# Kernel optimization log

Hardware: AMD Instinct MI355X
Metric: run time of the kernel (lower is better)

The kernel has to match this reference:

```python
import jax, jax.numpy as jnp
import numpy as np

NT, NM, E, EL = 400000, 40000, 400000, 1000000
C, H = 64, 64  # node_embedding_channels, hidden_channels
F_T = 384      # thesis feature dim


def setup_inputs() -> dict:
    key = jax.random.key(0)
    ks = jax.random.split(key, 24)
    s = 1.0 / np.sqrt(C)
    inp = {
        "x_thesis": jax.random.normal(ks[0], (NT, F_T), jnp.float32),
        "thesis_node_id": jnp.arange(NT, dtype=jnp.int32),
        "mentor_node_id": jnp.arange(NM, dtype=jnp.int32),
        "edge_src": jax.random.randint(ks[1], (E,), 0, NT, jnp.int32),
        "edge_dst": jax.random.randint(ks[2], (E,), 0, NM, jnp.int32),
        "el_src": jax.random.randint(ks[3], (EL,), 0, NT, jnp.int32),
        "el_dst": jax.random.randint(ks[4], (EL,), 0, NM, jnp.int32),
        "lin_W": jax.random.normal(ks[5], (C, F_T), jnp.float32) / np.sqrt(F_T),
        "lin_b": jnp.zeros((C,), jnp.float32),
        "emb_t": jax.random.normal(ks[6], (NT, C), jnp.float32),
        "emb_m": jax.random.normal(ks[7], (NM, C), jnp.float32),
        # SAGEConv params per layer per edge type (tm: thesis->mentor, mt: mentor->thesis)
        "Wl_tm0": jax.random.normal(ks[8], (H, C), jnp.float32) * s,
        "Wr_tm0": jax.random.normal(ks[9], (H, C), jnp.float32) * s,
        "b_tm0": jnp.zeros((H,), jnp.float32),
        "Wl_mt0": jax.random.normal(ks[10], (H, C), jnp.float32) * s,
        "Wr_mt0": jax.random.normal(ks[11], (H, C), jnp.float32) * s,
        "b_mt0": jnp.zeros((H,), jnp.float32),
        "Wl_tm1": jax.random.normal(ks[12], (H, H), jnp.float32) * s,
        "Wr_tm1": jax.random.normal(ks[13], (H, H), jnp.float32) * s,
        "b_tm1": jnp.zeros((H,), jnp.float32),
        "Wl_mt1": jax.random.normal(ks[14], (H, H), jnp.float32) * s,
        "Wr_mt1": jax.random.normal(ks[15], (H, H), jnp.float32) * s,
        "b_mt1": jnp.zeros((H,), jnp.float32),
    }
    return inp


def _segment_mean(msgs, seg_ids, num_segments):
    summed = jax.ops.segment_sum(msgs, seg_ids, num_segments=num_segments)
    cnt = jax.ops.segment_sum(jnp.ones((msgs.shape[0],), msgs.dtype), seg_ids,
                              num_segments=num_segments)
    return summed / jnp.maximum(cnt, 1.0)[:, None]


def _sage_layer(x_t, x_m, edge_src, edge_dst,
                Wl_tm, Wr_tm, b_tm, Wl_mt, Wr_mt, b_mt):
    # thesis -> mentor: mean-aggregate thesis neighbors at each mentor
    agg_m = _segment_mean(x_t[edge_src], edge_dst, x_m.shape[0])
    out_m = agg_m @ Wl_tm.T + x_m @ Wr_tm.T + b_tm
    # mentor -> thesis (reverse edges): mean-aggregate mentor neighbors at each thesis
    agg_t = _segment_mean(x_m[edge_dst], edge_src, x_t.shape[0])
    out_t = agg_t @ Wl_mt.T + x_t @ Wr_mt.T + b_mt
    return out_t, out_m


def reference(x_thesis, thesis_node_id, mentor_node_id, edge_src, edge_dst,
              el_src, el_dst, lin_W, lin_b, emb_t, emb_m,
              Wl_tm0, Wr_tm0, b_tm0, Wl_mt0, Wr_mt0, b_mt0,
              Wl_tm1, Wr_tm1, b_tm1, Wl_mt1, Wr_mt1, b_mt1):
    # node encoders
    x_t = x_thesis @ lin_W.T + lin_b + emb_t[thesis_node_id]
    x_m = emb_m[mentor_node_id]
    # 2-layer hetero GraphSAGE (ReLU between layers, none after last)
    x_t, x_m = _sage_layer(x_t, x_m, edge_src, edge_dst,
                           Wl_tm0, Wr_tm0, b_tm0, Wl_mt0, Wr_mt0, b_mt0)
    x_t, x_m = jax.nn.relu(x_t), jax.nn.relu(x_m)
    x_t, x_m = _sage_layer(x_t, x_m, edge_src, edge_dst,
                           Wl_tm1, Wr_tm1, b_tm1, Wl_mt1, Wr_mt1, b_mt1)
    # edge dot-product classifier over label edges
    return jnp.sum(x_t[el_src] * x_m[el_dst], axis=-1)
```

## Files before the change

kernel.cpp:

```cpp
#include <hip/hip_runtime.h>
#include <hip/hip_bf16.h>
#include <cstdint>
#include <cstddef>

#define TILE_BM 64
#define TILE_BN 64
#define TILE_BK 32

__global__ __launch_bounds__(256)
void encoder_kernel(const float* __restrict__ X, int K,
                    const float* __restrict__ W,
                    const float* __restrict__ bias,
                    const int* __restrict__ ids,
                    const float* __restrict__ emb,
                    float* __restrict__ out, int M)
{
    __shared__ float As[TILE_BK][TILE_BM + 4];
    __shared__ float Bs[TILE_BK][TILE_BN + 4];
    const int tid  = threadIdx.x;
    const int row0 = blockIdx.x * TILE_BM;
    const int tr   = tid >> 4;
    const int tc   = tid & 15;

    float acc[4][4];
#pragma unroll
    for (int i = 0; i < 4; i++)
#pragma unroll
        for (int j = 0; j < 4; j++) acc[i][j] = 0.f;

    for (int k0 = 0; k0 < K; k0 += TILE_BK) {
#pragma unroll
        for (int i = 0; i < 2; i++) {
            int idx = tid + i * 256;
            int r = idx >> 3;
            int j = idx & 7;
            int gr = row0 + r;
            float4 v = make_float4(0.f, 0.f, 0.f, 0.f);
            if (gr < M) v = *(const float4*)&X[(size_t)gr * K + k0 + j * 4];
            As[j * 4 + 0][r] = v.x; As[j * 4 + 1][r] = v.y;
            As[j * 4 + 2][r] = v.z; As[j * 4 + 3][r] = v.w;
        }
#pragma unroll
        for (int i = 0; i < 2; i++) {
            int idx = tid + i * 256;
            int c = idx >> 3;
            int j = idx & 7;
            float4 v = *(const float4*)&W[(size_t)c * K + k0 + j * 4];
            Bs[j * 4 + 0][c] = v.x; Bs[j * 4 + 1][c] = v.y;
            Bs[j * 4 + 2][c] = v.z; Bs[j * 4 + 3][c] = v.w;
        }
        __syncthreads();
#pragma unroll
        for (int kk = 0; kk < TILE_BK; kk++) {
            float4 av = *(const float4*)&As[kk][tr * 4];
            float4 bv = *(const float4*)&Bs[kk][tc * 4];
            float a_[4] = {av.x, av.y, av.z, av.w};
            float b_[4] = {bv.x, bv.y, bv.z, bv.w};
#pragma unroll
            for (int i = 0; i < 4; i++)
#pragma unroll
                for (int j = 0; j < 4; j++) acc[i][j] += a_[i] * b_[j];
        }
        __syncthreads();
    }

    float4 bv = *(const float4*)&bias[tc * 4];
#pragma unroll
    for (int i = 0; i < 4; i++) {
        int r = row0 + tr * 4 + i;
        if (r >= M) continue;
        int id = ids[r];
        float4 ev = *(const float4*)&emb[(size_t)id * 64 + tc * 4];
        float4 o;
        o.x = acc[i][0] + bv.x + ev.x;
        o.y = acc[i][1] + bv.y + ev.y;
        o.z = acc[i][2] + bv.z + ev.z;
        o.w = acc[i][3] + bv.w + ev.w;
        *(float4*)&out[(size_t)r * 64 + tc * 4] = o;
    }
}

__global__ __launch_bounds__(256)
void sage_linear_kernel(const float* __restrict__ A0, const float* __restrict__ W0,
                        const float* __restrict__ A1, const float* __restrict__ W1,
                        const float* __restrict__ bias, float* __restrict__ out,
                        int M, int relu)
{
    __shared__ float As[TILE_BK][TILE_BM + 4];
    __shared__ float Bs[TILE_BK][TILE_BN + 4];
    const int tid  = threadIdx.x;
    const int row0 = blockIdx.x * TILE_BM;
    const int tr   = tid >> 4;
    const int tc   = tid & 15;

    float acc[4][4];
#pragma unroll
    for (int i = 0; i < 4; i++)
#pragma unroll
        for (int j = 0; j < 4; j++) acc[i][j] = 0.f;

    for (int phase = 0; phase < 2; phase++) {
        const float* A = phase ? A1 : A0;
        const float* W = phase ? W1 : W0;
        for (int k0 = 0; k0 < 64; k0 += TILE_BK) {
#pragma unroll
            for (int i = 0; i < 2; i++) {
                int idx = tid + i * 256;
                int r = idx >> 3;
                int j = idx & 7;
                int gr = row0 + r;
                float4 v = make_float4(0.f, 0.f, 0.f, 0.f);
                if (gr < M) v = *(const float4*)&A[(size_t)gr * 64 + k0 + j * 4];
                As[j * 4 + 0][r] = v.x; As[j * 4 + 1][r] = v.y;
                As[j * 4 + 2][r] = v.z; As[j * 4 + 3][r] = v.w;
            }
#pragma unroll
            for (int i = 0; i < 2; i++) {
                int idx = tid + i * 256;
                int c = idx >> 3;
                int j = idx & 7;
                float4 v = *(const float4*)&W[(size_t)c * 64 + k0 + j * 4];
                Bs[j * 4 + 0][c] = v.x; Bs[j * 4 + 1][c] = v.y;
                Bs[j * 4 + 2][c] = v.z; Bs[j * 4 + 3][c] = v.w;
            }
            __syncthreads();
#pragma unroll
            for (int kk = 0; kk < TILE_BK; kk++) {
                float4 av = *(const float4*)&As[kk][tr * 4];
                float4 bv = *(const float4*)&Bs[kk][tc * 4];
                float a_[4] = {av.x, av.y, av.z, av.w};
                float b_[4] = {bv.x, bv.y, bv.z, bv.w};
#pragma unroll
                for (int i = 0; i < 4; i++)
#pragma unroll
                    for (int j = 0; j < 4; j++) acc[i][j] += a_[i] * b_[j];
            }
            __syncthreads();
        }
    }

    float4 bv = *(const float4*)&bias[tc * 4];
#pragma unroll
    for (int i = 0; i < 4; i++) {
        int r = row0 + tr * 4 + i;
        if (r >= M) continue;
        float4 o;
        o.x = acc[i][0] + bv.x;
        o.y = acc[i][1] + bv.y;
        o.z = acc[i][2] + bv.z;
        o.w = acc[i][3] + bv.w;
        if (relu) {
            o.x = fmaxf(o.x, 0.f); o.y = fmaxf(o.y, 0.f);
            o.z = fmaxf(o.z, 0.f); o.w = fmaxf(o.w, 0.f);
        }
        *(float4*)&out[(size_t)r * 64 + tc * 4] = o;
    }
}

__global__ void deg_kernel(const int* __restrict__ src, const int* __restrict__ dst,
                           float* __restrict__ deg_t, float* __restrict__ deg_m, int E)
{
    int e = blockIdx.x * 256 + threadIdx.x;
    if (e < E) {
        atomicAdd(&deg_t[src[e]], 1.f);
        atomicAdd(&deg_m[dst[e]], 1.f);
    }
}

__global__ void inv_kernel(float* __restrict__ d, int n)
{
    int i = blockIdx.x * 256 + threadIdx.x;
    if (i < n) d[i] = 1.f / fmaxf(d[i], 1.f);
}

__global__ void gather_rows_kernel(const float* __restrict__ src, const int* __restrict__ ids,
                                   float* __restrict__ out, int M)
{
    int gid = blockIdx.x * 256 + threadIdx.x;
    int r = gid >> 4;
    int j = gid & 15;
    if (r < M) {
        *(float4*)&out[(size_t)r * 64 + j * 4] =
            *(const float4*)&src[(size_t)ids[r] * 64 + j * 4];
    }
}

__global__ __launch_bounds__(256)
void scatter_kernel(const float* __restrict__ feat, const int* __restrict__ idx_from,
                    const int* __restrict__ idx_to, const float* __restrict__ inv_deg,
                    float* __restrict__ agg, int E)
{
    int gid = blockIdx.x * 256 + threadIdx.x;
    int e = gid >> 6;
    int c = gid & 63;
    if (e < E) {
        int f = idx_from[e];
        int t = idx_to[e];
        float v = feat[(size_t)f * 64 + c] * inv_deg[t];
        atomicAdd(&agg[(size_t)t * 64 + c], v);
    }
}

__global__ __launch_bounds__(256)
void classify_kernel(const float* __restrict__ xt, const float* __restrict__ xm,
                     const int* __restrict__ es, const int* __restrict__ ed,
                     float* __restrict__ out, int EL)
{
    int gid = blockIdx.x * 256 + threadIdx.x;
    int g = gid >> 4;
    int j = gid & 15;
    if (g < EL) {
        int s = es[g];
        int d = ed[g];
        float4 a = *(const float4*)&xt[(size_t)s * 64 + j * 4];
        float4 b = *(const float4*)&xm[(size_t)d * 64 + j * 4];
        float v = a.x * b.x + a.y * b.y + a.z * b.z + a.w * b.w;
        v += __shfl_down(v, 8, 16);
        v += __shfl_down(v, 4, 16);
        v += __shfl_down(v, 2, 16);
        v += __shfl_down(v, 1, 16);
        if (j == 0) out[g] = v;
    }
}

extern "C" void kernel_launch(void* const* d_in, const int* in_sizes, int n_in,
                              void* d_out, int out_size, void* d_ws, size_t ws_size,
                              hipStream_t stream)
{
    const float* x_thesis  = (const float*)d_in[0];
    const int*   thesis_id = (const int*)d_in[1];
    const int*   mentor_id = (const int*)d_in[2];
    const int*   edge_src  = (const int*)d_in[3];
    const int*   edge_dst  = (const int*)d_in[4];
    const int*   el_src    = (const int*)d_in[5];
    const int*   el_dst    = (const int*)d_in[6];
    const float* lin_W     = (const float*)d_in[7];
    const float* lin_b     = (const float*)d_in[8];
    const float* emb_t     = (const float*)d_in[9];
    const float* emb_m     = (const float*)d_in[10];
    const float* Wl_tm0    = (const float*)d_in[11];
    const float* Wr_tm0    = (const float*)d_in[12];
    const float* b_tm0     = (const float*)d_in[13];
    const float* Wl_mt0    = (const float*)d_in[14];
    const float* Wr_mt0    = (const float*)d_in[15];
    const float* b_mt0     = (const float*)d_in[16];
    const float* Wl_tm1    = (const float*)d_in[17];
    const float* Wr_tm1    = (const float*)d_in[18];
    const float* b_tm1     = (const float*)d_in[19];
    const float* Wl_mt1    = (const float*)d_in[20];
    const float* Wr_mt1    = (const float*)d_in[21];
    const float* b_mt1     = (const float*)d_in[22];

    const int NT = in_sizes[1];
    const int NM = in_sizes[2];
    const int E  = in_sizes[3];
    const int EL = in_sizes[5];
    const int FT = in_sizes[0] / NT;

    char* ws = (char*)d_ws;
    size_t off = 0;
    auto alloc = [&](size_t bytes) -> void* {
        void* p = ws + off;
        off += (bytes + 255) & ~(size_t)255;
        return p;
    };
    float* xt_a  = (float*)alloc((size_t)NT * 64 * 4);
    float* xt_b  = (float*)alloc((size_t)NT * 64 * 4);
    float* agg_t = (float*)alloc((size_t)NT * 64 * 4);
    float* xm_a  = (float*)alloc((size_t)NM * 64 * 4);
    float* xm_b  = (float*)alloc((size_t)NM * 64 * 4);
    float* agg_m = (float*)alloc((size_t)NM * 64 * 4);
    float* deg_t = (float*)alloc((size_t)NT * 4);
    float* deg_m = (float*)alloc((size_t)NM * 4);
    (void)ws_size; (void)n_in; (void)out_size;

    hipMemsetAsync(deg_t, 0, (size_t)NT * 4, stream);
    hipMemsetAsync(deg_m, 0, (size_t)NM * 4, stream);
    deg_kernel<<<(E + 255) / 256, 256, 0, stream>>>(edge_src, edge_dst, deg_t, deg_m, E);
    inv_kernel<<<(NT + 255) / 256, 256, 0, stream>>>(deg_t, NT);
    inv_kernel<<<(NM + 255) / 256, 256, 0, stream>>>(deg_m, NM);

    encoder_kernel<<<(NT + 63) / 64, 256, 0, stream>>>(x_thesis, FT, lin_W, lin_b,
                                                       thesis_id, emb_t, xt_a, NT);
    gather_rows_kernel<<<(NM * 16 + 255) / 256, 256, 0, stream>>>(emb_m, mentor_id, xm_a, NM);

    const int scatter_grid = (int)(((size_t)E * 64 + 255) / 256);

    hipMemsetAsync(agg_m, 0, (size_t)NM * 64 * 4, stream);
    hipMemsetAsync(agg_t, 0, (size_t)NT * 64 * 4, stream);
    scatter_kernel<<<scatter_grid, 256, 0, stream>>>(xt_a, edge_src, edge_dst, deg_m, agg_m, E);
    scatter_kernel<<<scatter_grid, 256, 0, stream>>>(xm_a, edge_dst, edge_src, deg_t, agg_t, E);
    sage_linear_kernel<<<(NM + 63) / 64, 256, 0, stream>>>(agg_m, Wl_tm0, xm_a, Wr_tm0,
                                                           b_tm0, xm_b, NM, 1);
    sage_linear_kernel<<<(NT + 63) / 64, 256, 0, stream>>>(agg_t, Wl_mt0, xt_a, Wr_mt0,
                                                           b_mt0, xt_b, NT, 1);

    hipMemsetAsync(agg_m, 0, (size_t)NM * 64 * 4, stream);
    hipMemsetAsync(agg_t, 0, (size_t)NT * 64 * 4, stream);
    scatter_kernel<<<scatter_grid, 256, 0, stream>>>(xt_b, edge_src, edge_dst, deg_m, agg_m, E);
    scatter_kernel<<<scatter_grid, 256, 0, stream>>>(xm_b, edge_dst, edge_src, deg_t, agg_t, E);
    sage_linear_kernel<<<(NM + 63) / 64, 256, 0, stream>>>(agg_m, Wl_tm1, xm_b, Wr_tm1,
                                                           b_tm1, xm_a, NM, 0);
    sage_linear_kernel<<<(NT + 63) / 64, 256, 0, stream>>>(agg_t, Wl_mt1, xt_b, Wr_mt1,
                                                           b_mt1, xt_a, NT, 0);

    classify_kernel<<<(int)(((size_t)EL * 16 + 255) / 256), 256, 0, stream>>>(
        xt_a, xm_a, el_src, el_dst, (float*)d_out, EL);
}
```

Baseline: 1.713 ms.

## Replace atomic scatter aggregation with CSR build and pull-based gather

Builds CSR adjacency for both directions (integer degree count, three-pass prefix scan, atomic-cursor fill), then computes each segment mean by having each destination row gather and sum its neighbours' features. This removes the per-element float atomics of the scatter kernels and the memsets of the aggregation buffers, and it folds the mean division into the gather. The cost is several extra small kernels and extra workspace for the CSR. Neighbour order inside a segment is nondeterministic, so the float summation order can vary between runs.

```diff
diff --git a/kernel.cpp b/kernel.cpp
--- a/kernel.cpp
+++ b/kernel.cpp
@@ -6,6 +6,7 @@
 #define TILE_BM 64
 #define TILE_BN 64
 #define TILE_BK 32
+#define SCAN_CHUNK 1024
 
 __global__ __launch_bounds__(256)
 void encoder_kernel(const float* __restrict__ X, int K,
@@ -157,20 +158,130 @@
     }
 }
 
-__global__ void deg_kernel(const int* __restrict__ src, const int* __restrict__ dst,
-                           float* __restrict__ deg_t, float* __restrict__ deg_m, int E)
+__global__ void deg_int_kernel(const int* __restrict__ src, const int* __restrict__ dst,
+                               int* __restrict__ deg_t, int* __restrict__ deg_m, int E)
 {
     int e = blockIdx.x * 256 + threadIdx.x;
     if (e < E) {
-        atomicAdd(&deg_t[src[e]], 1.f);
-        atomicAdd(&deg_m[dst[e]], 1.f);
-    }
-}
-
-__global__ void inv_kernel(float* __restrict__ d, int n)
-{
-    int i = blockIdx.x * 256 + threadIdx.x;
-    if (i < n) d[i] = 1.f / fmaxf(d[i], 1.f);
+        atomicAdd(&deg_t[src[e]], 1);
+        atomicAdd(&deg_m[dst[e]], 1);
+    }
+}
+
+__global__ __launch_bounds__(256)
+void scan1_kernel(const int* __restrict__ in, int* __restrict__ bsum, int n)
+{
+    __shared__ int lds[256];
+    const int base = blockIdx.x * SCAN_CHUNK;
+    const int t = threadIdx.x;
+    int s = 0;
+#pragma unroll
+    for (int i = 0; i < 4; i++) {
+        int idx = base + t * 4 + i;
+        if (idx < n) s += in[idx];
+    }
+    lds[t] = s;
+    __syncthreads();
+    for (int st = 128; st > 0; st >>= 1) {
+        if (t < st) lds[t] += lds[t + st];
+        __syncthreads();
+    }
+    if (t == 0) bsum[blockIdx.x] = lds[0];
+}
+
+__global__ __launch_bounds__(1024)
+void scan2_kernel(int* __restrict__ bsum, int nb)
+{
+    __shared__ int lds[1024];
+    const int t = threadIdx.x;
+    int v = (t < nb) ? bsum[t] : 0;
+    lds[t] = v;
+    __syncthreads();
+    int incl = v;
+    for (int st = 1; st < 1024; st <<= 1) {
+        int add = (t >= st) ? lds[t - st] : 0;
+        __syncthreads();
+        incl += add;
+        lds[t] = incl;
+        __syncthreads();
+    }
+    if (t < nb) bsum[t] = incl - v;
+}
+
+__global__ __launch_bounds__(256)
+void scan3_kernel(const int* __restrict__ in, const int* __restrict__ bsum,
+                  int* __restrict__ off, int* __restrict__ cur, int n)
+{
+    __shared__ int lds[256];
+    const int base = blockIdx.x * SCAN_CHUNK;
+    const int t = threadIdx.x;
+    int v[4];
+    int s = 0;
+#pragma unroll
+    for (int i = 0; i < 4; i++) {
+        int idx = base + t * 4 + i;
+        v[i] = (idx < n) ? in[idx] : 0;
+        s += v[i];
+    }
+    lds[t] = s;
+    __syncthreads();
+    int incl = s;
+    for (int st = 1; st < 256; st <<= 1) {
+        int add = (t >= st) ? lds[t - st] : 0;
+        __syncthreads();
+        incl += add;
+        lds[t] = incl;
+        __syncthreads();
+    }
+    int run = incl - s + bsum[blockIdx.x];
+#pragma unroll
+    for (int i = 0; i < 4; i++) {
+        int idx = base + t * 4 + i;
+        if (idx < n) {
+            off[idx] = run;
+            cur[idx] = run;
+            run += v[i];
+        }
+    }
+}
+
+__global__ void csr_fill_kernel(const int* __restrict__ src, const int* __restrict__ dst,
+                                int* __restrict__ curT, int* __restrict__ curM,
+                                int* __restrict__ colT, int* __restrict__ colM, int E)
+{
+    int e = blockIdx.x * 256 + threadIdx.x;
+    if (e < E) {
+        int s = src[e];
+        int d = dst[e];
+        int pt = atomicAdd(&curT[s], 1);
+        colT[pt] = d;
+        int pm = atomicAdd(&curM[d], 1);
+        colM[pm] = s;
+    }
+}
+
+__global__ __launch_bounds__(256)
+void agg_gather_kernel(const float* __restrict__ feat, const int* __restrict__ off,
+                       const int* __restrict__ deg, const int* __restrict__ col,
+                       float* __restrict__ out, int M)
+{
+    int gid = blockIdx.x * 256 + threadIdx.x;
+    int r = gid >> 6;
+    int c = gid & 63;
+    if (r >= M) return;
+    int o = off[r];
+    int d = deg[r];
+    float acc0 = 0.f, acc1 = 0.f;
+    int i = 0;
+    for (; i + 2 <= d; i += 2) {
+        int c0 = col[o + i];
+        int c1 = col[o + i + 1];
+        acc0 += feat[(size_t)c0 * 64 + c];
+        acc1 += feat[(size_t)c1 * 64 + c];
+    }
+    if (i < d) acc0 += feat[(size_t)col[o + i] * 64 + c];
+    float inv = 1.f / (float)max(d, 1);
+    out[(size_t)r * 64 + c] = (acc0 + acc1) * inv;
 }
 
 __global__ void gather_rows_kernel(const float* __restrict__ src, const int* __restrict__ ids,
@@ -182,22 +293,6 @@
     if (r < M) {
         *(float4*)&out[(size_t)r * 64 + j * 4] =
             *(const float4*)&src[(size_t)ids[r] * 64 + j * 4];
-    }
-}
-
-__global__ __launch_bounds__(256)
-void scatter_kernel(const float* __restrict__ feat, const int* __restrict__ idx_from,
-                    const int* __restrict__ idx_to, const float* __restrict__ inv_deg,
-                    float* __restrict__ agg, int E)
-{
-    int gid = blockIdx.x * 256 + threadIdx.x;
-    int e = gid >> 6;
-    int c = gid & 63;
-    if (e < E) {
-        int f = idx_from[e];
-        int t = idx_to[e];
-        float v = feat[(size_t)f * 64 + c] * inv_deg[t];
-        atomicAdd(&agg[(size_t)t * 64 + c], v);
     }
 }
 
@@ -270,35 +365,49 @@
     float* xm_a  = (float*)alloc((size_t)NM * 64 * 4);
     float* xm_b  = (float*)alloc((size_t)NM * 64 * 4);
     float* agg_m = (float*)alloc((size_t)NM * 64 * 4);
-    float* deg_t = (float*)alloc((size_t)NT * 4);
-    float* deg_m = (float*)alloc((size_t)NM * 4);
+    int*   deg_t = (int*)alloc((size_t)NT * 4);
+    int*   deg_m = (int*)alloc((size_t)NM * 4);
+    int*   off_t = (int*)alloc((size_t)NT * 4);
+    int*   cur_t = (int*)alloc((size_t)NT * 4);
+    int*   off_m = (int*)alloc((size_t)NM * 4);
+    int*   cur_m = (int*)alloc((size_t)NM * 4);
+    int*   col_t = (int*)alloc((size_t)E * 4);
+    int*   col_m = (int*)alloc((size_t)E * 4);
+    int*   bsum_t = (int*)alloc((size_t)1024 * 4);
+    int*   bsum_m = (int*)alloc((size_t)1024 * 4);
     (void)ws_size; (void)n_in; (void)out_size;
+
+    const int nbT = (NT + SCAN_CHUNK - 1) / SCAN_CHUNK;
+    const int nbM = (NM + SCAN_CHUNK - 1) / SCAN_CHUNK;
 
     hipMemsetAsync(deg_t, 0, (size_t)NT * 4, stream);
     hipMemsetAsync(deg_m, 0, (size_t)NM * 4, stream);
-    deg_kernel<<<(E + 255) / 256, 256, 0, stream>>>(edge_src, edge_dst, deg_t, deg_m, E);
-    inv_kernel<<<(NT + 255) / 256, 256, 0, stream>>>(deg_t, NT);
-    inv_kernel<<<(NM + 255) / 256, 256, 0, stream>>>(deg_m, NM);
+    deg_int_kernel<<<(E + 255) / 256, 256, 0, stream>>>(edge_src, edge_dst, deg_t, deg_m, E);
+    scan1_kernel<<<nbT, 256, 0, stream>>>(deg_t, bsum_t, NT);
+    scan2_kernel<<<1, 1024, 0, stream>>>(bsum_t, nbT);
+    scan3_kernel<<<nbT, 256, 0, stream>>>(deg_t, bsum_t, off_t, cur_t, NT);
+    scan1_kernel<<<nbM, 256, 0, stream>>>(deg_m, bsum_m, NM);
+    scan2_kernel<<<1, 1024, 0, stream>>>(bsum_m, nbM);
+    scan3_kernel<<<nbM, 256, 0, stream>>>(deg_m, bsum_m, off_m, cur_m, NM);
+    csr_fill_kernel<<<(E + 255) / 256, 256, 0, stream>>>(edge_src, edge_dst,
+                                                         cur_t, cur_m, col_t, col_m, E);
 
     encoder_kernel<<<(NT + 63) / 64, 256, 0, stream>>>(x_thesis, FT, lin_W, lin_b,
                                                        thesis_id, emb_t, xt_a, NT);
     gather_rows_kernel<<<(NM * 16 + 255) / 256, 256, 0, stream>>>(emb_m, mentor_id, xm_a, NM);
 
-    const int scatter_grid = (int)(((size_t)E * 64 + 255) / 256);
-
-    hipMemsetAsync(agg_m, 0, (size_t)NM * 64 * 4, stream);
-    hipMemsetAsync(agg_t, 0, (size_t)NT * 64 * 4, stream);
-    scatter_kernel<<<scatter_grid, 256, 0, stream>>>(xt_a, edge_src, edge_dst, deg_m, agg_m, E);
-    scatter_kernel<<<scatter_grid, 256, 0, stream>>>(xm_a, edge_dst, edge_src, deg_t, agg_t, E);
+    const int gridAggT = (int)(((size_t)NT * 64 + 255) / 256);
+    const int gridAggM = (int)(((size_t)NM * 64 + 255) / 256);
+
+    agg_gather_kernel<<<gridAggM, 256, 0, stream>>>(xt_a, off_m, deg_m, col_m, agg_m, NM);
+    agg_gather_kernel<<<gridAggT, 256, 0, stream>>>(xm_a, off_t, deg_t, col_t, agg_t, NT);
     sage_linear_kernel<<<(NM + 63) / 64, 256, 0, stream>>>(agg_m, Wl_tm0, xm_a, Wr_tm0,
                                                            b_tm0, xm_b, NM, 1);
     sage_linear_kernel<<<(NT + 63) / 64, 256, 0, stream>>>(agg_t, Wl_mt0, xt_a, Wr_mt0,
                                                            b_mt0, xt_b, NT, 1);
 
-    hipMemsetAsync(agg_m, 0, (size_t)NM * 64 * 4, stream);
-    hipMemsetAsync(agg_t, 0, (size_t)NT * 64 * 4, stream);
-    scatter_kernel<<<scatter_grid, 256, 0, stream>>>(xt_b, edge_src, edge_dst, deg_m, agg_m, E);
-    scatter_kernel<<<scatter_grid, 256, 0, stream>>>(xm_b, edge_dst, edge_src, deg_t, agg_t, E);
+    agg_gather_kernel<<<gridAggM, 256, 0, stream>>>(xt_b, off_m, deg_m, col_m, agg_m, NM);
+    agg_gather_kernel<<<gridAggT, 256, 0, stream>>>(xm_b, off_t, deg_t, col_t, agg_t, NT);
     sage_linear_kernel<<<(NM + 63) / 64, 256, 0, stream>>>(agg_m, Wl_tm1, xm_b, Wr_tm1,
                                                            b_tm1, xm_a, NM, 0);
     sage_linear_kernel<<<(NT + 63) / 64, 256, 0, stream>>>(agg_t, Wl_mt1, xt_b, Wr_mt1,
```

New measurement: 1.612 ms. -5.9%, faster.
